# Optimization experiments

Hardware: AMD Instinct MI355X
Metric: run time of the kernel (lower is better)

The kernel has to match this reference:

```python
import jax, jax.numpy as jnp
import numpy as np
import itertools

B, N, C, D = 2, 150000, 64, 128  # samples, points/sample, channels, voxel grid extent
EPS = 1e-4  # BatchNormBlock eps
# 3x3x3 submanifold kernel offsets (27 taps)
OFFS = jnp.array(list(itertools.product((-1, 0, 1), repeat=3)), dtype=jnp.int32)  # [27,3]


def setup_inputs() -> dict:
    key = jax.random.key(0)
    k1, k2 = jax.random.split(key)
    rng = np.random.default_rng(0)
    # unique voxel coordinates per sample on a D^3 grid
    pos = np.stack([
        np.stack(np.unravel_index(rng.choice(D ** 3, size=N, replace=False), (D, D, D)), axis=-1)
        for _ in range(B)
    ]).astype(np.int32)  # [B,N,3]
    feats = jax.random.normal(k1, (B, N, C), jnp.float32)
    # 4 submanifold convs (2 residual blocks x 2 convs), fan-in scaled
    Ws = jax.random.normal(k2, (4, 27, C, C), jnp.float32) / np.sqrt(27 * C)
    gammas = jnp.ones((4, C), jnp.float32)
    betas = jnp.zeros((4, C), jnp.float32)
    return {"feats": feats, "Ws": Ws, "gammas": gammas, "betas": betas, "pos": jnp.asarray(pos)}


def _build_lut(pos_b):  # pos_b: [N,3] int32 -> dense hash grid [D^3] of point index or -1
    code = (pos_b[:, 0] * D + pos_b[:, 1]) * D + pos_b[:, 2]
    return jnp.full((D ** 3,), -1, jnp.int32).at[code].set(jnp.arange(N, dtype=jnp.int32))


def _subconv(x, lut_b, pos_b, W):
    # submanifold sparse conv: per kernel tap, gather neighbor features and GEMM
    # x:[N,C], lut_b:[D^3], pos_b:[N,3], W:[27,Cin,Cout]
    def step(acc, kw):
        d, Wk = kw
        npos = pos_b + d  # [N,3]
        valid = jnp.all((npos >= 0) & (npos < D), axis=-1)
        code = (npos[:, 0] * D + npos[:, 1]) * D + npos[:, 2]
        nidx = lut_b[jnp.where(valid, code, 0)]
        valid = valid & (nidx >= 0)
        g = jnp.where(valid[:, None], x[jnp.clip(nidx, 0, N - 1)], 0.0)  # [N,Cin]
        return acc + g @ Wk, None

    acc0 = jnp.zeros((x.shape[0], W.shape[-1]), x.dtype)
    acc, _ = jax.lax.scan(step, acc0, (OFFS, W))
    return acc


def _bn_relu(x, g, b):
    # BatchNormBlock (train mode, biased var over all concatenated points) + ReLU
    mu = x.mean(axis=(0, 1))
    var = jnp.mean(jnp.square(x - mu), axis=(0, 1))
    return jax.nn.relu((x - mu) * jax.lax.rsqrt(var + EPS) * g + b)


def reference(feats, Ws, gammas, betas, pos):
    lut = jax.vmap(_build_lut)(pos)  # [B, D^3]
    conv = jax.vmap(_subconv, in_axes=(0, 0, 0, None))
    x = feats
    for blk in range(2):  # conv_block_reps ResidualBlocks (NIN is Identity since nIn==nOut)
        out1 = x
        h = _bn_relu(x, gammas[2 * blk], betas[2 * blk])
        h = conv(h, lut, pos, Ws[2 * blk])
        h = _bn_relu(h, gammas[2 * blk + 1], betas[2 * blk + 1])
        out2 = conv(h, lut, pos, Ws[2 * blk + 1])
        x = out1 + out2
    return x
```

## Files before the change

kernel.cpp:

```cpp
#include <hip/hip_runtime.h>
#include <stdint.h>

#define DGRID 128
#define D3 (DGRID * DGRID * DGRID)
#define NBATCH 2
#define NPTS 150000
#define NROWS (NBATCH * NPTS)
#define NPAD 300032
#define ZROW NROWS
#define NCBLK (NPAD / 128)
#define NCELLS 8192
#define EPSBN 1e-4f
#define SBLK 1024

typedef __attribute__((ext_vector_type(8))) short s16x8;
typedef __attribute__((ext_vector_type(4))) float f32x4;

static __device__ __forceinline__ uint32_t f2bf_rne(float f) {
  uint32_t b = __float_as_uint(f);
  return (b + 0x7FFFu + ((b >> 16) & 1u)) >> 16;
}

static __device__ __forceinline__ f32x4 mfma16(uint4 a, uint4 b, f32x4 c) {
  return __builtin_amdgcn_mfma_f32_16x16x32_bf16(
      __builtin_bit_cast(s16x8, a), __builtin_bit_cast(s16x8, b), c, 0, 0, 0);
}

__global__ void k_scatter(const int* __restrict__ pos, int* __restrict__ lut) {
  int g = blockIdx.x * blockDim.x + threadIdx.x;
  if (g >= NROWS) return;
  int b = g / NPTS;
  int i = g - b * NPTS;
  int x = pos[3 * g], y = pos[3 * g + 1], z = pos[3 * g + 2];
  lut[(size_t)b * D3 + (x * DGRID + y) * DGRID + z] = i;
}

__global__ void k_cellcount(const int* __restrict__ pos, int* __restrict__ cnt) {
  int g = blockIdx.x * blockDim.x + threadIdx.x;
  if (g >= NROWS) return;
  int b = g / NPTS;
  int cid = (b << 12) | ((pos[3 * g] >> 3) << 8) | ((pos[3 * g + 1] >> 3) << 4) |
            (pos[3 * g + 2] >> 3);
  atomicAdd(&cnt[cid], 1);
}

__global__ void k_scan(const int* __restrict__ cnt, int* __restrict__ cstart) {
  __shared__ int s[1024];
  int tid = threadIdx.x;
  int e[8];
  int sum = 0;
#pragma unroll
  for (int j = 0; j < 8; j++) {
    int v = cnt[tid * 8 + j];
    e[j] = sum;
    sum += v;
  }
  s[tid] = sum;
  __syncthreads();
  for (int off = 1; off < 1024; off <<= 1) {
    int t = (tid >= off) ? s[tid - off] : 0;
    __syncthreads();
    s[tid] += t;
    __syncthreads();
  }
  int base = tid ? s[tid - 1] : 0;
#pragma unroll
  for (int j = 0; j < 8; j++) cstart[tid * 8 + j] = base + e[j];
}

__global__ void k_bucket(const int* __restrict__ pos, const int* __restrict__ cstart,
                         int* __restrict__ fill, int* __restrict__ perm,
                         int* __restrict__ iperm) {
  int g = blockIdx.x * blockDim.x + threadIdx.x;
  if (g >= NROWS) return;
  int b = g / NPTS;
  int cid = (b << 12) | ((pos[3 * g] >> 3) << 8) | ((pos[3 * g + 1] >> 3) << 4) |
            (pos[3 * g + 2] >> 3);
  int slot = cstart[cid] + atomicAdd(&fill[cid], 1);
  perm[slot] = g;
  iperm[g] = slot;
}

__global__ void k_nbr_s(const int* __restrict__ pos, const int* __restrict__ lut,
                        const int* __restrict__ perm, const int* __restrict__ iperm,
                        int* __restrict__ nbr) {
  int s = blockIdx.x * blockDim.x + threadIdx.x;
  if (s >= NPAD) return;
  if (s >= NROWS) {
#pragma unroll
    for (int t = 0; t < 27; ++t) nbr[(size_t)t * NPAD + s] = ZROW;
    return;
  }
  int g = perm[s];
  int b = g / NPTS;
  int x = pos[3 * g], y = pos[3 * g + 1], z = pos[3 * g + 2];
  const int* L = lut + (size_t)b * D3;
  const int* ip = iperm + (size_t)b * NPTS;
#pragma unroll
  for (int t = 0; t < 27; ++t) {
    int nx = x + t / 9 - 1;
    int ny = y + (t / 3) % 3 - 1;
    int nz = z + t % 3 - 1;
    int v = ZROW;
    if ((unsigned)nx < DGRID && (unsigned)ny < DGRID && (unsigned)nz < DGRID) {
      int n = L[(nx * DGRID + ny) * DGRID + nz];
      if (n >= 0) v = ip[n];
    }
    nbr[(size_t)t * NPAD + s] = v;
  }
}

__global__ void k_wpack(const float* __restrict__ Ws, uint4* __restrict__ Wfrag) {
  int e = blockIdx.x * 256 + threadIdx.x;
  if (e >= 4 * 27 * 512) return;
  int lane = e & 63, nb = (e >> 6) & 3, s = (e >> 8) & 1, tt = e >> 9;
  int kb = s * 32 + (lane >> 4) * 8;
  int cout = nb * 16 + (lane & 15);
  const float* src = Ws + (size_t)tt * 4096;
  uint32_t p[4];
#pragma unroll
  for (int j = 0; j < 4; ++j) {
    uint32_t lo = f2bf_rne(src[(kb + 2 * j) * 64 + cout]);
    uint32_t hi = f2bf_rne(src[(kb + 2 * j + 1) * 64 + cout]);
    p[j] = (hi << 16) | lo;
  }
  uint4 o;
  o.x = p[0]; o.y = p[1]; o.z = p[2]; o.w = p[3];
  Wfrag[e] = o;
}

__global__ void k_stats1(const float* __restrict__ X, float* __restrict__ part) {
  __shared__ float s[512];
  int c = threadIdx.x & 63, q = threadIdx.x >> 6;
  float sm = 0.f, sq = 0.f;
  for (int r = blockIdx.x * 4 + q; r < NROWS; r += SBLK * 4) {
    float v = X[(size_t)r * 64 + c];
    sm += v;
    sq += v * v;
  }
  s[threadIdx.x] = sm;
  s[256 + threadIdx.x] = sq;
  __syncthreads();
  if (q == 0) {
    sm = s[c] + s[64 + c] + s[128 + c] + s[192 + c];
    sq = s[256 + c] + s[320 + c] + s[384 + c] + s[448 + c];
    part[blockIdx.x * 128 + c] = sm;
    part[blockIdx.x * 128 + 64 + c] = sq;
  }
}

__global__ void k_stats2(const float* __restrict__ part, int nblk,
                         const float* __restrict__ gamma, const float* __restrict__ beta,
                         float* __restrict__ chanp, int cid) {
  __shared__ float s[512];
  int c = threadIdx.x & 63, q = threadIdx.x >> 6;
  float sm = 0.f, sq = 0.f;
  for (int rb = q; rb < nblk; rb += 4) {
    sm += part[rb * 128 + c];
    sq += part[rb * 128 + 64 + c];
  }
  s[threadIdx.x] = sm;
  s[256 + threadIdx.x] = sq;
  __syncthreads();
  if (q == 0) {
    sm = s[c] + s[64 + c] + s[128 + c] + s[192 + c];
    sq = s[256 + c] + s[320 + c] + s[384 + c] + s[448 + c];
    float mean = sm / (float)NROWS;
    float var = sq / (float)NROWS - mean * mean;
    float a = gamma[cid * 64 + c] * rsqrtf(var + EPSBN);
    chanp[cid * 128 + c] = a;
    chanp[cid * 128 + 64 + c] = beta[cid * 64 + c] - mean * a;
  }
}

__global__ void k_hpass(const float* __restrict__ X, const float* __restrict__ chanp,
                        int cid, const int* __restrict__ gperm, uint4* __restrict__ h) {
  int g = blockIdx.x * blockDim.x + threadIdx.x;
  if (g >= (NROWS + 1) * 8) return;
  int row = g >> 3;
  if (row >= NROWS) {
    h[g] = (uint4){0u, 0u, 0u, 0u};
    return;
  }
  int src = gperm ? gperm[row] : row;
  int c0 = (g & 7) * 8;
  const float* cp = chanp + cid * 128;
  const float4 a0 = *(const float4*)(cp + c0);
  const float4 a1 = *(const float4*)(cp + c0 + 4);
  const float4 b0 = *(const float4*)(cp + 64 + c0);
  const float4 b1 = *(const float4*)(cp + 64 + c0 + 4);
  const float* Xr = X + (size_t)src * 64 + c0;
  const float4 x0 = *(const float4*)Xr;
  const float4 x1 = *(const float4*)(Xr + 4);
  float v0 = fmaxf(fmaf(x0.x, a0.x, b0.x), 0.f);
  float v1 = fmaxf(fmaf(x0.y, a0.y, b0.y), 0.f);
  float v2 = fmaxf(fmaf(x0.z, a0.z, b0.z), 0.f);
  float v3 = fmaxf(fmaf(x0.w, a0.w, b0.w), 0.f);
  float v4 = fmaxf(fmaf(x1.x, a1.x, b1.x), 0.f);
  float v5 = fmaxf(fmaf(x1.y, a1.y, b1.y), 0.f);
  float v6 = fmaxf(fmaf(x1.z, a1.z, b1.z), 0.f);
  float v7 = fmaxf(fmaf(x1.w, a1.w, b1.w), 0.f);
  uint4 o;
  o.x = (f2bf_rne(v1) << 16) | f2bf_rne(v0);
  o.y = (f2bf_rne(v3) << 16) | f2bf_rne(v2);
  o.z = (f2bf_rne(v5) << 16) | f2bf_rne(v4);
  o.w = (f2bf_rne(v7) << 16) | f2bf_rne(v6);
  h[g] = o;
}

#define PH(T, WU, WL, AU, AL, NIU, NIL)                                     \
  {                                                                         \
    int tw = (T) + 1 <= 26 ? (T) + 1 : 26;                                  \
    const uint4* Wt = Wf + (size_t)tw * 512 + lane;                         \
    _Pragma("unroll") for (int i = 0; i < 8; i++) WL[i] = Wt[i * 64];       \
    int tn = (T) + 4 <= 26 ? (T) + 4 : 26;                                  \
    _Pragma("unroll") for (int rt = 0; rt < 2; rt++)                        \
        NIL[rt] = nbp[(size_t)tn * NPAD + rt * 16];                         \
    {                                                                       \
      const uint4* hp0 = h + (size_t)NIU[0] * 8 + lkg;                      \
      const uint4* hp1 = h + (size_t)NIU[1] * 8 + lkg;                      \
      AL[0][0] = hp0[0]; AL[0][1] = hp0[4];                                 \
      AL[1][0] = hp1[0]; AL[1][1] = hp1[4];                                 \
    }                                                                       \
    _Pragma("unroll") for (int s = 0; s < 2; s++)                           \
      _Pragma("unroll") for (int rt = 0; rt < 2; rt++)                      \
        _Pragma("unroll") for (int nb = 0; nb < 4; nb++)                    \
          acc[rt][nb] = mfma16(AU[rt][s], WU[s * 4 + nb], acc[rt][nb]);     \
  }

__global__ __launch_bounds__(256, 2) void k_conv(
    const uint4* __restrict__ h, const uint4* __restrict__ Wf,
    const int* __restrict__ nbr, const float* __restrict__ res,
    const int* __restrict__ rperm, float* __restrict__ out,
    const int* __restrict__ wperm, float* __restrict__ part, int do_stats) {
  __shared__ float xp[4][16 * 68];
  __shared__ float sred[2][4][4][16];
  int tid = threadIdx.x, wv = tid >> 6, lane = tid & 63;
  int tbase = (blockIdx.x * 4 + wv) * 32;
  int lrow = lane & 15, lkg = lane >> 4;

  f32x4 acc[2][4];
#pragma unroll
  for (int i = 0; i < 2; i++)
#pragma unroll
    for (int j = 0; j < 4; j++) acc[i][j] = (f32x4){0.f, 0.f, 0.f, 0.f};

  const int* nbp = nbr + tbase + lrow;
  int niA[2], niB[2], niC[2];
  uint4 wA[8], wB[8], wC[8];
  uint4 aA[2][2], aB[2][2], aC[2][2];

  int p0[2], p1[2];
#pragma unroll
  for (int i = 0; i < 8; i++) wA[i] = Wf[i * 64 + lane];
#pragma unroll
  for (int rt = 0; rt < 2; rt++) p0[rt] = nbp[rt * 16];
#pragma unroll
  for (int rt = 0; rt < 2; rt++) p1[rt] = nbp[(size_t)NPAD + rt * 16];
#pragma unroll
  for (int rt = 0; rt < 2; rt++) niA[rt] = nbp[(size_t)2 * NPAD + rt * 16];
#pragma unroll
  for (int rt = 0; rt < 2; rt++) niB[rt] = nbp[(size_t)3 * NPAD + rt * 16];
  {
    const uint4* hp0 = h + (size_t)p0[0] * 8 + lkg;
    const uint4* hp1 = h + (size_t)p0[1] * 8 + lkg;
    aA[0][0] = hp0[0]; aA[0][1] = hp0[4];
    aA[1][0] = hp1[0]; aA[1][1] = hp1[4];
  }
  {
    const uint4* hp0 = h + (size_t)p1[0] * 8 + lkg;
    const uint4* hp1 = h + (size_t)p1[1] * 8 + lkg;
    aB[0][0] = hp0[0]; aB[0][1] = hp0[4];
    aB[1][0] = hp1[0]; aB[1][1] = hp1[4];
  }

  for (int t = 0; t < 27; t += 3) {
    PH(t, wA, wB, aA, aC, niA, niC)
    PH(t + 1, wB, wC, aB, aA, niB, niA)
    PH(t + 2, wC, wA, aC, aB, niC, niB)
  }

  float smc[16], sqc[16];
#pragma unroll
  for (int j = 0; j < 16; j++) smc[j] = sqc[j] = 0.f;
  float* slab = xp[wv];
#pragma unroll 1
  for (int rt = 0; rt < 2; rt++) {
#pragma unroll
    for (int nb = 0; nb < 4; nb++)
#pragma unroll
      for (int r = 0; r < 4; r++)
        slab[(lkg * 4 + r) * 68 + nb * 16 + lrow] = acc[rt][nb][r];
    __syncthreads();
    int gr = tbase + rt * 16 + lrow;
    if (gr < NROWS) {
      int rowr = rperm ? rperm[gr] : gr;
      int roww = wperm ? wperm[gr] : gr;
#pragma unroll
      for (int j = 0; j < 4; j++) {
        float4 vv = *(float4*)&slab[lrow * 68 + lkg * 16 + j * 4];
        size_t cofs = (size_t)(lkg * 16 + j * 4);
        if (res) {
          float4 rr = *(const float4*)(res + (size_t)rowr * 64 + cofs);
          vv.x += rr.x; vv.y += rr.y; vv.z += rr.z; vv.w += rr.w;
        }
        *(float4*)(out + (size_t)roww * 64 + cofs) = vv;
        smc[j * 4 + 0] += vv.x; sqc[j * 4 + 0] += vv.x * vv.x;
        smc[j * 4 + 1] += vv.y; sqc[j * 4 + 1] += vv.y * vv.y;
        smc[j * 4 + 2] += vv.z; sqc[j * 4 + 2] += vv.z * vv.z;
        smc[j * 4 + 3] += vv.w; sqc[j * 4 + 3] += vv.w * vv.w;
      }
    }
    __syncthreads();
  }
  if (do_stats) {
#pragma unroll
    for (int j = 0; j < 16; j++) {
      smc[j] += __shfl_xor(smc[j], 1); sqc[j] += __shfl_xor(sqc[j], 1);
      smc[j] += __shfl_xor(smc[j], 2); sqc[j] += __shfl_xor(sqc[j], 2);
      smc[j] += __shfl_xor(smc[j], 4); sqc[j] += __shfl_xor(sqc[j], 4);
      smc[j] += __shfl_xor(smc[j], 8); sqc[j] += __shfl_xor(sqc[j], 8);
    }
    if (lrow == 0) {
#pragma unroll
      for (int j = 0; j < 16; j++) {
        sred[0][wv][lkg][j] = smc[j];
        sred[1][wv][lkg][j] = sqc[j];
      }
    }
    __syncthreads();
    if (tid < 64) {
      float s0 = 0.f, s1 = 0.f;
      int q = tid >> 4, c = tid & 15;
#pragma unroll
      for (int w = 0; w < 4; w++) {
        s0 += sred[0][w][q][c];
        s1 += sred[1][w][q][c];
      }
      part[blockIdx.x * 128 + tid] = s0;
      part[blockIdx.x * 128 + 64 + tid] = s1;
    }
  }
}

extern "C" void kernel_launch(void* const* d_in, const int* in_sizes, int n_in,
                              void* d_out, int out_size, void* d_ws, size_t ws_size,
                              hipStream_t stream) {
  const float* feats = (const float*)d_in[0];
  const float* Ws = (const float*)d_in[1];
  const float* gammas = (const float*)d_in[2];
  const float* betas = (const float*)d_in[3];
  const int* pos = (const int*)d_in[4];
  float* out = (float*)d_out;

  char* w = (char*)d_ws;
  auto alloc = [&](size_t b) {
    char* p = w;
    w += (b + 255) & ~(size_t)255;
    return p;
  };
  int* nbr = (int*)alloc((size_t)27 * NPAD * 4);
  uint4* Wfrag = (uint4*)alloc((size_t)4 * 27 * 512 * 16);
  float* part = (float*)alloc((size_t)NCBLK * 128 * 4);
  float* chanp = (float*)alloc((size_t)4 * 128 * 4);
  int* perm = (int*)alloc((size_t)NPAD * 4);
  int* iperm = (int*)alloc((size_t)NROWS * 4);
  int* ccnt = (int*)alloc((size_t)NCELLS * 4);
  int* cfill = (int*)alloc((size_t)NCELLS * 4);
  int* cstart = (int*)alloc((size_t)NCELLS * 4);
  uint4* h = (uint4*)alloc((size_t)NPAD * 128);
  float* xbuf = (float*)alloc((size_t)NROWS * 64 * 4);
  char* reg0 = alloc((size_t)NROWS * 64 * 4);
  float* cbuf = (float*)reg0;
  int* lut = (int*)reg0;

  hipMemsetAsync(lut, 0xFF, (size_t)NBATCH * D3 * 4, stream);
  hipMemsetAsync(ccnt, 0, (size_t)NCELLS * 8, stream);
  int gpts = (NROWS + 255) / 256;
  k_scatter<<<gpts, 256, 0, stream>>>(pos, lut);
  k_cellcount<<<gpts, 256, 0, stream>>>(pos, ccnt);
  k_scan<<<1, 1024, 0, stream>>>(ccnt, cstart);
  k_bucket<<<gpts, 256, 0, stream>>>(pos, cstart, cfill, perm, iperm);
  k_nbr_s<<<NPAD / 256, 256, 0, stream>>>(pos, lut, perm, iperm, nbr);
  k_wpack<<<216, 256, 0, stream>>>(Ws, Wfrag);

  k_stats1<<<SBLK, 256, 0, stream>>>(feats, part);
  k_stats2<<<1, 256, 0, stream>>>(part, SBLK, gammas, betas, chanp, 0);
  k_hpass<<<9376, 256, 0, stream>>>(feats, chanp, 0, perm, h);
  k_conv<<<NCBLK, 256, 0, stream>>>(h, Wfrag + 0 * 27 * 512, nbr, nullptr, nullptr,
                                    cbuf, nullptr, part, 1);

  k_stats2<<<1, 256, 0, stream>>>(part, NCBLK, gammas, betas, chanp, 1);
  k_hpass<<<9376, 256, 0, stream>>>(cbuf, chanp, 1, nullptr, h);
  k_conv<<<NCBLK, 256, 0, stream>>>(h, Wfrag + 1 * 27 * 512, nbr, feats, perm,
                                    xbuf, nullptr, part, 1);

  k_stats2<<<1, 256, 0, stream>>>(part, NCBLK, gammas, betas, chanp, 2);
  k_hpass<<<9376, 256, 0, stream>>>(xbuf, chanp, 2, nullptr, h);
  k_conv<<<NCBLK, 256, 0, stream>>>(h, Wfrag + 2 * 27 * 512, nbr, nullptr, nullptr,
                                    cbuf, nullptr, part, 1);

  k_stats2<<<1, 256, 0, stream>>>(part, NCBLK, gammas, betas, chanp, 3);
  k_hpass<<<9376, 256, 0, stream>>>(cbuf, chanp, 3, nullptr, h);
  k_conv<<<NCBLK, 256, 0, stream>>>(h, Wfrag + 3 * 27 * 512, nbr, xbuf, nullptr,
                                    out, perm, part, 0);
}
```

Before: 1.363 ms.

## Stage conv weights in LDS per tap group and shrink gather prefetch pipeline

Each block now cooperatively copies the weights for four taps into shared memory, with barriers between groups, and every wave reads its weight fragments from LDS. Before, each wave loaded the weights from global memory into a triple-buffered register set. The gather prefetch drops from three rotating buffers to two, and the 2-blocks-per-SM launch bound is removed. These changes are meant to cut register pressure and redundant global weight traffic, at the cost of extra barriers and LDS reads in the tap loop. The epilogue is also remapped so each lane writes contiguous channels of one row and the stats shuffle reduction is simpler.

After: 1.738 ms. 27.5% more time.

```diff
diff --git a/kernel.cpp b/kernel.cpp
--- a/kernel.cpp
+++ b/kernel.cpp
@@ -208,33 +208,34 @@
   h[g] = o;
 }
 
-#define PH(T, WU, WL, AU, AL, NIU, NIL)                                     \
+#define PHASE(KS, T, AC, NIC)                                               \
   {                                                                         \
-    int tw = (T) + 1 <= 26 ? (T) + 1 : 26;                                  \
-    const uint4* Wt = Wf + (size_t)tw * 512 + lane;                         \
-    _Pragma("unroll") for (int i = 0; i < 8; i++) WL[i] = Wt[i * 64];       \
-    int tn = (T) + 4 <= 26 ? (T) + 4 : 26;                                  \
-    _Pragma("unroll") for (int rt = 0; rt < 2; rt++)                        \
-        NIL[rt] = nbp[(size_t)tn * NPAD + rt * 16];                         \
-    {                                                                       \
-      const uint4* hp0 = h + (size_t)NIU[0] * 8 + lkg;                      \
-      const uint4* hp1 = h + (size_t)NIU[1] * 8 + lkg;                      \
-      AL[0][0] = hp0[0]; AL[0][1] = hp0[4];                                 \
-      AL[1][0] = hp1[0]; AL[1][1] = hp1[4];                                 \
-    }                                                                       \
+    uint4 wf[8];                                                            \
+    _Pragma("unroll") for (int i = 0; i < 8; i++)                           \
+        wf[i] = wlds[(KS) * 512 + i * 64 + lane];                           \
     _Pragma("unroll") for (int s = 0; s < 2; s++)                           \
       _Pragma("unroll") for (int rt = 0; rt < 2; rt++)                      \
         _Pragma("unroll") for (int nb = 0; nb < 4; nb++)                    \
-          acc[rt][nb] = mfma16(AU[rt][s], WU[s * 4 + nb], acc[rt][nb]);     \
-  }
-
-__global__ __launch_bounds__(256, 2) void k_conv(
+          acc[rt][nb] = mfma16(AC[rt][s], wf[s * 4 + nb], acc[rt][nb]);     \
+    {                                                                       \
+      const uint4* hp0 = h + (size_t)NIC[0] * 8 + lkg;                      \
+      const uint4* hp1 = h + (size_t)NIC[1] * 8 + lkg;                      \
+      AC[0][0] = hp0[0]; AC[0][1] = hp0[4];                                 \
+      AC[1][0] = hp1[0]; AC[1][1] = hp1[4];                                 \
+    }                                                                       \
+    int tn = (T) + 4 <= 26 ? (T) + 4 : 26;                                  \
+    NIC[0] = nbp[(size_t)tn * NPAD];                                        \
+    NIC[1] = nbp[(size_t)tn * NPAD + 16];                                   \
+  }
+
+__global__ __launch_bounds__(256) void k_conv(
     const uint4* __restrict__ h, const uint4* __restrict__ Wf,
     const int* __restrict__ nbr, const float* __restrict__ res,
     const int* __restrict__ rperm, float* __restrict__ out,
     const int* __restrict__ wperm, float* __restrict__ part, int do_stats) {
-  __shared__ float xp[4][16 * 68];
-  __shared__ float sred[2][4][4][16];
+  __shared__ uint4 smem4[2048];
+  uint4* wlds = smem4;
+  char* smem = (char*)smem4;
   int tid = threadIdx.x, wv = tid >> 6, lane = tid & 63;
   int tbase = (blockIdx.x * 4 + wv) * 32;
   int lrow = lane & 15, lkg = lane >> 4;
@@ -246,44 +247,43 @@
     for (int j = 0; j < 4; j++) acc[i][j] = (f32x4){0.f, 0.f, 0.f, 0.f};
 
   const int* nbp = nbr + tbase + lrow;
-  int niA[2], niB[2], niC[2];
-  uint4 wA[8], wB[8], wC[8];
-  uint4 aA[2][2], aB[2][2], aC[2][2];
-
-  int p0[2], p1[2];
-#pragma unroll
-  for (int i = 0; i < 8; i++) wA[i] = Wf[i * 64 + lane];
-#pragma unroll
-  for (int rt = 0; rt < 2; rt++) p0[rt] = nbp[rt * 16];
-#pragma unroll
-  for (int rt = 0; rt < 2; rt++) p1[rt] = nbp[(size_t)NPAD + rt * 16];
-#pragma unroll
-  for (int rt = 0; rt < 2; rt++) niA[rt] = nbp[(size_t)2 * NPAD + rt * 16];
-#pragma unroll
-  for (int rt = 0; rt < 2; rt++) niB[rt] = nbp[(size_t)3 * NPAD + rt * 16];
+  int niE[2], niO[2];
+  uint4 aE[2][2], aO[2][2];
   {
-    const uint4* hp0 = h + (size_t)p0[0] * 8 + lkg;
-    const uint4* hp1 = h + (size_t)p0[1] * 8 + lkg;
-    aA[0][0] = hp0[0]; aA[0][1] = hp0[4];
-    aA[1][0] = hp1[0]; aA[1][1] = hp1[4];
-  }
-  {
-    const uint4* hp0 = h + (size_t)p1[0] * 8 + lkg;
-    const uint4* hp1 = h + (size_t)p1[1] * 8 + lkg;
-    aB[0][0] = hp0[0]; aB[0][1] = hp0[4];
-    aB[1][0] = hp1[0]; aB[1][1] = hp1[4];
-  }
-
-  for (int t = 0; t < 27; t += 3) {
-    PH(t, wA, wB, aA, aC, niA, niC)
-    PH(t + 1, wB, wC, aB, aA, niB, niA)
-    PH(t + 2, wC, wA, aC, aB, niC, niB)
-  }
-
-  float smc[16], sqc[16];
-#pragma unroll
-  for (int j = 0; j < 16; j++) smc[j] = sqc[j] = 0.f;
-  float* slab = xp[wv];
+    int q0 = nbp[0], q1 = nbp[16];
+    int r0 = nbp[NPAD], r1 = nbp[NPAD + 16];
+    niE[0] = nbp[(size_t)2 * NPAD]; niE[1] = nbp[(size_t)2 * NPAD + 16];
+    niO[0] = nbp[(size_t)3 * NPAD]; niO[1] = nbp[(size_t)3 * NPAD + 16];
+    const uint4* hp0 = h + (size_t)q0 * 8 + lkg;
+    const uint4* hp1 = h + (size_t)q1 * 8 + lkg;
+    aE[0][0] = hp0[0]; aE[0][1] = hp0[4];
+    aE[1][0] = hp1[0]; aE[1][1] = hp1[4];
+    const uint4* hp2 = h + (size_t)r0 * 8 + lkg;
+    const uint4* hp3 = h + (size_t)r1 * 8 + lkg;
+    aO[0][0] = hp2[0]; aO[0][1] = hp2[4];
+    aO[1][0] = hp3[0]; aO[1][1] = hp3[4];
+  }
+
+  for (int g = 0; g < 7; g++) {
+    int t0 = g * 4;
+    int nt = (27 - t0 >= 4) ? 4 : 27 - t0;
+    __syncthreads();
+#pragma unroll 2
+    for (int c = wv; c < nt * 8; c += 4) {
+      uint4 v = Wf[(size_t)t0 * 512 + c * 64 + lane];
+      *(uint4*)(smem + (size_t)c * 1024 + lane * 16) = v;
+    }
+    __syncthreads();
+    PHASE(0, t0, aE, niE)
+    if (nt > 1) PHASE(1, t0 + 1, aO, niO)
+    if (nt > 2) PHASE(2, t0 + 2, aE, niE)
+    if (nt > 3) PHASE(3, t0 + 3, aO, niO)
+  }
+
+  float sm4[4] = {0.f, 0.f, 0.f, 0.f}, sq4[4] = {0.f, 0.f, 0.f, 0.f};
+  float* slab = (float*)smem + wv * 1088;
+  float* sred = (float*)(smem + 17408);
+  __syncthreads();
 #pragma unroll 1
   for (int rt = 0; rt < 2; rt++) {
 #pragma unroll
@@ -292,50 +292,47 @@
       for (int r = 0; r < 4; r++)
         slab[(lkg * 4 + r) * 68 + nb * 16 + lrow] = acc[rt][nb][r];
     __syncthreads();
-    int gr = tbase + rt * 16 + lrow;
-    if (gr < NROWS) {
-      int rowr = rperm ? rperm[gr] : gr;
-      int roww = wperm ? wperm[gr] : gr;
-#pragma unroll
-      for (int j = 0; j < 4; j++) {
-        float4 vv = *(float4*)&slab[lrow * 68 + lkg * 16 + j * 4];
-        size_t cofs = (size_t)(lkg * 16 + j * 4);
+#pragma unroll
+    for (int j = 0; j < 4; j++) {
+      int row = tbase + rt * 16 + j * 4 + lkg;
+      if (row < NROWS) {
+        float4 vv = *(float4*)&slab[(j * 4 + lkg) * 68 + lrow * 4];
+        size_t cofs = (size_t)lrow * 4;
         if (res) {
-          float4 rr = *(const float4*)(res + (size_t)rowr * 64 + cofs);
-          vv.x += rr.x; vv.y += rr.y; vv.z += rr.z; vv.w += rr.w;
+          int rr = rperm ? rperm[row] : row;
+          float4 rv = *(const float4*)(res + (size_t)rr * 64 + cofs);
+          vv.x += rv.x; vv.y += rv.y; vv.z += rv.z; vv.w += rv.w;
         }
-        *(float4*)(out + (size_t)roww * 64 + cofs) = vv;
-        smc[j * 4 + 0] += vv.x; sqc[j * 4 + 0] += vv.x * vv.x;
-        smc[j * 4 + 1] += vv.y; sqc[j * 4 + 1] += vv.y * vv.y;
-        smc[j * 4 + 2] += vv.z; sqc[j * 4 + 2] += vv.z * vv.z;
-        smc[j * 4 + 3] += vv.w; sqc[j * 4 + 3] += vv.w * vv.w;
+        int rw = wperm ? wperm[row] : row;
+        *(float4*)(out + (size_t)rw * 64 + cofs) = vv;
+        sm4[0] += vv.x; sq4[0] += vv.x * vv.x;
+        sm4[1] += vv.y; sq4[1] += vv.y * vv.y;
+        sm4[2] += vv.z; sq4[2] += vv.z * vv.z;
+        sm4[3] += vv.w; sq4[3] += vv.w * vv.w;
       }
     }
     __syncthreads();
   }
   if (do_stats) {
 #pragma unroll
-    for (int j = 0; j < 16; j++) {
-      smc[j] += __shfl_xor(smc[j], 1); sqc[j] += __shfl_xor(sqc[j], 1);
-      smc[j] += __shfl_xor(smc[j], 2); sqc[j] += __shfl_xor(sqc[j], 2);
-      smc[j] += __shfl_xor(smc[j], 4); sqc[j] += __shfl_xor(sqc[j], 4);
-      smc[j] += __shfl_xor(smc[j], 8); sqc[j] += __shfl_xor(sqc[j], 8);
-    }
-    if (lrow == 0) {
-#pragma unroll
-      for (int j = 0; j < 16; j++) {
-        sred[0][wv][lkg][j] = smc[j];
-        sred[1][wv][lkg][j] = sqc[j];
+    for (int k = 0; k < 4; k++) {
+      sm4[k] += __shfl_xor(sm4[k], 16); sq4[k] += __shfl_xor(sq4[k], 16);
+      sm4[k] += __shfl_xor(sm4[k], 32); sq4[k] += __shfl_xor(sq4[k], 32);
+    }
+    if (lane < 16) {
+#pragma unroll
+      for (int k = 0; k < 4; k++) {
+        sred[wv * 64 + lane * 4 + k] = sm4[k];
+        sred[256 + wv * 64 + lane * 4 + k] = sq4[k];
       }
     }
     __syncthreads();
     if (tid < 64) {
       float s0 = 0.f, s1 = 0.f;
-      int q = tid >> 4, c = tid & 15;
 #pragma unroll
       for (int w = 0; w < 4; w++) {
-        s0 += sred[0][w][q][c];
-        s1 += sred[1][w][q][c];
+        s0 += sred[w * 64 + tid];
+        s1 += sred[256 + w * 64 + tid];
       }
       part[blockIdx.x * 128 + tid] = s0;
       part[blockIdx.x * 128 + 64 + tid] = s1;
```
